# Kernel tuning notes

Measured on AMD Instinct MI355X. Metric: run time of the kernel, lower is better.

## Reference

```python
import jax, jax.numpy as jnp
import numpy as np


def _interp_bilinear_ac(x, out_h, out_w):
    """Bilinear resize with align_corners=True, NCHW."""
    n, c, h, w = x.shape
    ys = jnp.linspace(0.0, h - 1.0, out_h)
    xs = jnp.linspace(0.0, w - 1.0, out_w)
    y0 = jnp.floor(ys).astype(jnp.int32)
    y1 = jnp.minimum(y0 + 1, h - 1)
    wy = (ys - y0.astype(x.dtype))[None, None, :, None]
    x0 = jnp.floor(xs).astype(jnp.int32)
    x1 = jnp.minimum(x0 + 1, w - 1)
    wx = (xs - x0.astype(x.dtype))[None, None, None, :]
    # interpolate along H then W
    xh = x[:, :, y0, :] * (1.0 - wy) + x[:, :, y1, :] * wy  # [n,c,out_h,w]
    out = xh[:, :, :, x0] * (1.0 - wx) + xh[:, :, :, x1] * wx  # [n,c,out_h,out_w]
    return out


def setup_inputs() -> dict:
    key = jax.random.key(0)
    ks = jax.random.split(key, 7)
    return {
        "aspp": jax.random.normal(ks[0], (8, 128, 32, 32), jnp.float32),
        "f3": jax.random.normal(ks[1], (8, 128, 32, 32), jnp.float32),
        "inp": jax.random.normal(ks[2], (8, 4, 512, 512), jnp.float32),
        "cam": jax.random.normal(ks[3], (8, 21, 64, 64), jnp.float32),
        "w_aspp": jax.random.normal(ks[4], (64, 128), jnp.float32) * 0.05,
        "w_f3": jax.random.normal(ks[5], (64, 128), jnp.float32) * 0.05,
        "w_f9": jax.random.normal(ks[6], (128, 132), jnp.float32) * 0.05,
    }


def reference(aspp, f3, inp, cam, w_aspp, w_f3, w_f9):
    n, c, h, w = cam.shape
    # 1x1 convs (no bias) as channel matmuls
    f3p = jnp.einsum('oc,nchw->nohw', w_f3, f3)
    asppp = jnp.einsum('oc,nchw->nohw', w_aspp, aspp)
    # bilinear upsample (align_corners=True) to cam resolution
    asppp = _interp_bilinear_ac(asppp, h, w)
    x_s = _interp_bilinear_ac(inp, h, w)
    f3p = _interp_bilinear_ac(f3p, h, w)
    f = jnp.concatenate([x_s, asppp, f3p], axis=1)  # [n,132,h,w]
    f = jnp.einsum('oc,nchw->nohw', w_f9, f)        # [n,128,h,w]
    f = f.reshape(n, -1, h * w)                     # [n,128,hw]
    f = f / (jnp.linalg.norm(f, axis=1, keepdims=True) + 1e-5)
    # affinity: [n, hw, hw]
    aff = jax.nn.relu(jnp.einsum('ncp,ncq->npq', f, f))
    aff = aff / (jnp.sum(aff, axis=1, keepdims=True) + 1e-5)
    cam_rv = jnp.matmul(cam.reshape(n, -1, h * w), aff).reshape(n, -1, h, w)
    return cam_rv
```

## Files before the change

### kernel.cpp

```cpp
#include <hip/hip_runtime.h>
#include <math.h>

typedef unsigned short u16;
typedef unsigned int u32;
typedef __attribute__((ext_vector_type(8))) short bf16x8;
typedef __attribute__((ext_vector_type(4))) short short4v;
typedef __attribute__((ext_vector_type(4))) float f32x4;
typedef __attribute__((ext_vector_type(16))) float f32x16;

#define HW32 1024
#define HW64 4096
#define KCAM 21
#define PB 64
#define PSPLIT 4
#define FT_STR 168

#define GLOAD_LDS16(gsrc, ldst)                                                \
  __builtin_amdgcn_global_load_lds(                                            \
      (const __attribute__((address_space(1))) void*)(gsrc),                   \
      (__attribute__((address_space(3))) void*)(ldst), 16, 0, 0)

static __device__ __forceinline__ u16 f2bf(float x) {
  u32 u = __float_as_uint(x);
  u32 r = (u + 0x7FFFu + ((u >> 16) & 1u)) >> 16;
  return (u16)r;
}
static __device__ __forceinline__ float bf2f(u16 h) {
  return __uint_as_float(((u32)h) << 16);
}

__global__ __launch_bounds__(256) void k_conv32(
    const float* __restrict__ aspp, const float* __restrict__ f3,
    const float* __restrict__ w_aspp, const float* __restrict__ w_f3,
    const float* __restrict__ w_f9,
    float* __restrict__ a32, float* __restrict__ g32,
    u16* __restrict__ whi, u16* __restrict__ wlo)
{
  const int pt = blockIdx.x, which = blockIdx.y >> 2, jq = blockIdx.y & 3,
            n = blockIdx.z;

  if (blockIdx.y == 0) {
    const int bid = blockIdx.z * 4 + blockIdx.x;
#pragma unroll
    for (int k = 0; k < 3; ++k) {
      const int idx = bid * 256 + threadIdx.x + k * 8192;
      if (idx < 128 * 160) {
        const int o = idx / 160, c = idx - o * 160;
        const float v = (c < 132) ? w_f9[o * 132 + c] : 0.f;
        const u16 h = f2bf(v);
        whi[idx] = h;
        wlo[idx] = f2bf(v - bf2f(h));
      }
    }
  }

  const float* x = (which == 0 ? aspp : f3) + (size_t)n * 128 * HW32;
  const float* w = (which == 0 ? w_aspp : w_f3) + jq * 16 * 128;
  float* out = (which == 0 ? a32 : g32) + (size_t)n * 64 * HW32 + (size_t)jq * 16 * HW32;

  __shared__ __align__(16) float wlds[16 * 128];
  for (int i = threadIdx.x; i < 16 * 128; i += 256) wlds[i] = w[i];
  __syncthreads();

  const int p = pt * 256 + threadIdx.x;
  float acc[16];
#pragma unroll
  for (int j = 0; j < 16; ++j) acc[j] = 0.f;

  for (int c0 = 0; c0 < 128; c0 += 8) {
    float xv[8];
#pragma unroll
    for (int cc = 0; cc < 8; ++cc) xv[cc] = x[(size_t)(c0 + cc) * HW32 + p];
#pragma unroll
    for (int j = 0; j < 16; ++j) {
      const float4 w0 = *reinterpret_cast<const float4*>(&wlds[j * 128 + c0]);
      const float4 w1 = *reinterpret_cast<const float4*>(&wlds[j * 128 + c0 + 4]);
      acc[j] = fmaf(w0.x, xv[0], acc[j]);
      acc[j] = fmaf(w0.y, xv[1], acc[j]);
      acc[j] = fmaf(w0.z, xv[2], acc[j]);
      acc[j] = fmaf(w0.w, xv[3], acc[j]);
      acc[j] = fmaf(w1.x, xv[4], acc[j]);
      acc[j] = fmaf(w1.y, xv[5], acc[j]);
      acc[j] = fmaf(w1.z, xv[6], acc[j]);
      acc[j] = fmaf(w1.w, xv[7], acc[j]);
    }
  }
  for (int j = 0; j < 16; ++j) out[(size_t)j * HW32 + p] = acc[j];
}

__global__ __launch_bounds__(512) void k_build_f(
    const float* __restrict__ inp, const float* __restrict__ a32,
    const float* __restrict__ g32, const u16* __restrict__ whi,
    const u16* __restrict__ wlo, const float* __restrict__ cam,
    u16* __restrict__ fhi_g, u16* __restrict__ camA)
{
  const int y2 = blockIdx.x, n = blockIdx.y;
  const int tid = threadIdx.x;

  __shared__ __align__(16) u16 feat[128 * FT_STR];
  __shared__ __align__(16) u16 wh[128 * FT_STR];
  __shared__ __align__(16) u16 wl[128 * FT_STR];

  for (int ch = tid; ch < 2560; ch += 512) {
    const int o = ch / 20, c8 = (ch - o * 20) * 8;
    *(bf16x8*)&wh[o * FT_STR + c8] = *(const bf16x8*)(whi + o * 160 + c8);
    *(bf16x8*)&wl[o * FT_STR + c8] = *(const bf16x8*)(wlo + o * 160 + c8);
  }

  {
    u16* dst = camA + ((size_t)n * 32 + y2) * HW64;
    if (y2 < KCAM) {
      const float* src = cam + ((size_t)n * KCAM + y2) * HW64;
      for (int i = tid; i < HW64; i += 512) dst[i] = f2bf(src[i]);
    } else {
      const u16 v = (y2 == KCAM) ? f2bf(1.f) : (u16)0;
      for (int i = tid; i < HW64; i += 512) dst[i] = v;
    }
  }

  const float s512 = 511.f / 63.f, s32 = 31.f / 63.f;
  const int yA0i = y2 * 2, yA1i = y2 * 2 + 1;
  const float sA0 = yA0i * s512, sA1 = yA1i * s512;
  const int y0A0 = (int)sA0, y0A1 = (int)sA1;
  const float wyA0 = sA0 - y0A0, wyA1 = sA1 - y0A1;
  const int y1A0 = min(y0A0 + 1, 511), y1A1 = min(y0A1 + 1, 511);
  const float sB0 = yA0i * s32, sB1 = yA1i * s32;
  const int y0B0 = (int)sB0, y0B1 = (int)sB1;
  const float wyB0 = sB0 - y0B0, wyB1 = sB1 - y0B1;
  const int y1B0 = min(y0B0 + 1, 31), y1B1 = min(y0B1 + 1, 31);

  for (int idx = tid; idx < 132 * 128; idx += 512) {
    const int c = idx >> 7;
    const int pos = idx & 127;
    const int ly = pos >> 6, x = pos & 63;
    const int y0A = ly ? y0A1 : y0A0, y1A = ly ? y1A1 : y1A0;
    const float wyA = ly ? wyA1 : wyA0;
    const int y0B = ly ? y0B1 : y0B0, y1B = ly ? y1B1 : y1B0;
    const float wyB = ly ? wyB1 : wyB0;
    float v;
    if (c < 4) {
      const float sx = x * s512;
      const int x0 = (int)sx;
      const float wx = sx - (float)x0;
      const int x1 = min(x0 + 1, 511);
      const float* im = inp + (size_t)(n * 4 + c) * 512 * 512;
      const float v00 = im[y0A * 512 + x0], v01 = im[y0A * 512 + x1];
      const float v10 = im[y1A * 512 + x0], v11 = im[y1A * 512 + x1];
      v = (v00 * (1.f - wx) + v01 * wx) * (1.f - wyA) +
          (v10 * (1.f - wx) + v11 * wx) * wyA;
    } else {
      const float* im = (c < 68) ? a32 + (size_t)(n * 64 + (c - 4)) * HW32
                                 : g32 + (size_t)(n * 64 + (c - 68)) * HW32;
      const float sx = x * s32;
      const int x0 = (int)sx;
      const float wx = sx - (float)x0;
      const int x1 = min(x0 + 1, 31);
      const float v00 = im[y0B * 32 + x0], v01 = im[y0B * 32 + x1];
      const float v10 = im[y1B * 32 + x0], v11 = im[y1B * 32 + x1];
      v = (v00 * (1.f - wx) + v01 * wx) * (1.f - wyB) +
          (v10 * (1.f - wx) + v11 * wx) * wyB;
    }
    feat[pos * FT_STR + c] = f2bf(v);
  }
  for (int idx = tid; idx < 28 * 128; idx += 512) {
    const int c = 132 + (idx >> 7), pos = idx & 127;
    feat[pos * FT_STR + c] = 0;
  }
  __syncthreads();

  const int lane = tid & 63, wave = tid >> 6;
  const int l15 = lane & 15, l4 = lane >> 4;

  float acc[8][4];
#pragma unroll
  for (int m = 0; m < 8; ++m)
#pragma unroll
    for (int i = 0; i < 4; ++i) acc[m][i] = 0.f;

#pragma unroll
  for (int s = 0; s < 5; ++s) {
    const bf16x8 B =
        *(const bf16x8*)&feat[(wave * 16 + l15) * FT_STR + s * 32 + l4 * 8];
#pragma unroll
    for (int m = 0; m < 8; ++m) {
      const int wo = (m * 16 + l15) * FT_STR + s * 32 + l4 * 8;
      const bf16x8 Ahi = *(const bf16x8*)&wh[wo];
      const bf16x8 Alo = *(const bf16x8*)&wl[wo];
      f32x4 a = {acc[m][0], acc[m][1], acc[m][2], acc[m][3]};
      a = __builtin_amdgcn_mfma_f32_16x16x32_bf16(Ahi, B, a, 0, 0, 0);
      a = __builtin_amdgcn_mfma_f32_16x16x32_bf16(Alo, B, a, 0, 0, 0);
      acc[m][0] = a[0]; acc[m][1] = a[1]; acc[m][2] = a[2]; acc[m][3] = a[3];
    }
  }

  {
    float ss = 0.f;
#pragma unroll
    for (int m = 0; m < 8; ++m)
#pragma unroll
      for (int i = 0; i < 4; ++i) ss = fmaf(acc[m][i], acc[m][i], ss);
    ss += __shfl_xor(ss, 16);
    ss += __shfl_xor(ss, 32);
    const float inv = 1.f / (sqrtf(ss) + 1e-5f);
    const int pos = wave * 16 + l15;
    u16* fp = fhi_g + ((size_t)n * HW64 + (size_t)(y2 * 2 + (pos >> 6)) * 64 +
                       (pos & 63)) * 128 + l4 * 4;
#pragma unroll
    for (int m = 0; m < 8; ++m) {
      const float v0 = acc[m][0] * inv, v1 = acc[m][1] * inv;
      const float v2 = acc[m][2] * inv, v3 = acc[m][3] * inv;
      union { u32 d[2]; short4v h; } P;
      asm("v_cvt_pk_bf16_f32 %0, %1, %2" : "=v"(P.d[0]) : "v"(v0), "v"(v1));
      asm("v_cvt_pk_bf16_f32 %0, %1, %2" : "=v"(P.d[1]) : "v"(v2), "v"(v3));
      *(short4v*)(fp + m * 16) = P.h;
    }
  }
}

__global__ __launch_bounds__(256) void k_fused(
    const u16* __restrict__ fhi_g, const u16* __restrict__ camA,
    float* __restrict__ part)
{
  __shared__ __align__(16) u16 fh[2][PB * 128];

  const int gx = blockIdx.x;
  const int n = gx & 7;
  const int rest = gx >> 3;
  const int qt = rest & 15;
  const int ps = rest >> 4;
  const int tid = threadIdx.x;
  const int lane = tid & 63;
  const int wq = tid >> 6;
  const int l31 = lane & 31;
  const int lh = lane >> 5;
  const int qb = qt * 256;

  const u16* fbase = fhi_g + (size_t)n * HW64 * 128;

  bf16x8 Bq[2][8];
#pragma unroll
  for (int qh = 0; qh < 2; ++qh) {
    const size_t rowo = (size_t)(qb + wq * 64 + qh * 32 + l31) * 128;
#pragma unroll
    for (int ks = 0; ks < 8; ++ks)
      Bq[qh][ks] = *(const bf16x8*)(fbase + rowo + ks * 16 + lh * 8);
  }

  f32x16 nacc0, nacc1;
#pragma unroll
  for (int i = 0; i < 16; ++i) { nacc0[i] = 0.f; nacc1[i] = 0.f; }

  const int p_base = ps * (HW64 / PSPLIT);
  const int xorr = (l31 & 7) << 4;

  const int srow0 = (lane >> 4);
  const int scbl = (lane & 15) * 16;

#pragma unroll
  for (int s = 0; s < 4; ++s) {
    const int rr = (wq * 4 + s) * 4 + srow0;
    const u16* gsrc = fbase + (size_t)(p_base + rr) * 128 +
                      ((scbl ^ ((rr & 7) << 4)) >> 1);
    GLOAD_LDS16(gsrc, &fh[0][(wq * 4 + s) * 512]);
  }

  int cur = 0;
  for (int t = 0; t < (HW64 / PSPLIT) / PB; ++t) {
    const int p0 = p_base + t * PB;
    __syncthreads();

    if (t < 15) {
#pragma unroll
      for (int s = 0; s < 4; ++s) {
        const int rr = (wq * 4 + s) * 4 + srow0;
        const u16* gsrc = fbase + (size_t)(p0 + PB + rr) * 128 +
                          ((scbl ^ ((rr & 7) << 4)) >> 1);
        GLOAD_LDS16(gsrc, &fh[cur ^ 1][(wq * 4 + s) * 512]);
      }
    }

    bf16x8 Ac[4];
#pragma unroll
    for (int kst = 0; kst < 4; ++kst) {
      union { short4v h[2]; bf16x8 v; } A;
      const u16* cp = camA + ((size_t)n * 32 + l31) * HW64 + p0 + kst * 16 + lh * 4;
      A.h[0] = *(const short4v*)cp;
      A.h[1] = *(const short4v*)(cp + 8);
      Ac[kst] = A.v;
    }

    f32x16 accS[2][2];
#pragma unroll
    for (int ks = 0; ks < 8; ++ks) {
      const int cb = (ks * 32 + (lh << 4)) ^ xorr;
      bf16x8 Ah[2];
#pragma unroll
      for (int mt = 0; mt < 2; ++mt)
        Ah[mt] = *(const bf16x8*)&fh[cur][(mt * 32 + l31) * 128 + (cb >> 1)];
      if (ks == 0) {
        f32x16 z;
#pragma unroll
        for (int i = 0; i < 16; ++i) z[i] = 0.f;
#pragma unroll
        for (int mt = 0; mt < 2; ++mt) {
          accS[mt][0] = __builtin_amdgcn_mfma_f32_32x32x16_bf16(Ah[mt], Bq[0][0], z, 0, 0, 0);
          accS[mt][1] = __builtin_amdgcn_mfma_f32_32x32x16_bf16(Ah[mt], Bq[1][0], z, 0, 0, 0);
        }
      } else {
#pragma unroll
        for (int mt = 0; mt < 2; ++mt) {
          accS[mt][0] = __builtin_amdgcn_mfma_f32_32x32x16_bf16(Ah[mt], Bq[0][ks], accS[mt][0], 0, 0, 0);
          accS[mt][1] = __builtin_amdgcn_mfma_f32_32x32x16_bf16(Ah[mt], Bq[1][ks], accS[mt][1], 0, 0, 0);
        }
      }
    }

#pragma unroll
    for (int kst = 0; kst < 4; ++kst) {
      const int mt = kst >> 1, h8 = (kst & 1) * 8;
#pragma unroll
      for (int qh = 0; qh < 2; ++qh) {
        union { u32 d[4]; bf16x8 v; } W;
#pragma unroll
        for (int i = 0; i < 4; ++i) {
          const float a0 = fmaxf(accS[mt][qh][h8 + 2 * i], 0.f);
          const float a1 = fmaxf(accS[mt][qh][h8 + 2 * i + 1], 0.f);
          asm("v_cvt_pk_bf16_f32 %0, %1, %2" : "=v"(W.d[i]) : "v"(a0), "v"(a1));
        }
        if (qh == 0)
          nacc0 = __builtin_amdgcn_mfma_f32_32x32x16_bf16(Ac[kst], W.v, nacc0, 0, 0, 0);
        else
          nacc1 = __builtin_amdgcn_mfma_f32_32x32x16_bf16(Ac[kst], W.v, nacc1, 0, 0, 0);
      }
    }

    cur ^= 1;
  }

#pragma unroll
  for (int qh = 0; qh < 2; ++qh) {
    const int qg = qb + wq * 64 + qh * 32 + l31;
#pragma unroll
    for (int r = 0; r < 16; ++r) {
      const int row = (r & 3) + 8 * (r >> 2) + 4 * lh;
      if (row < 22)
        part[(((size_t)n * PSPLIT + ps) * 22 + row) * HW64 + qg] =
            (qh == 0) ? nacc0[r] : nacc1[r];
    }
  }
}

__global__ __launch_bounds__(256) void k_final(
    const float* __restrict__ part, float* __restrict__ out, int total4)
{
  const int idx = blockIdx.x * 256 + threadIdx.x;
  if (idx >= total4) return;
  const int n = idx / (KCAM * 1024);
  const int r = idx - n * (KCAM * 1024);
  const int k = r >> 10;
  const int q4 = (r & 1023) * 4;
  const float* base = part + (size_t)n * PSPLIT * 22 * HW64;
  float4 num = {0.f, 0.f, 0.f, 0.f}, den = {0.f, 0.f, 0.f, 0.f};
#pragma unroll
  for (int p = 0; p < PSPLIT; ++p) {
    const float4 nv = *reinterpret_cast<const float4*>(
        &base[((size_t)p * 22 + k) * HW64 + q4]);
    const float4 dv = *reinterpret_cast<const float4*>(
        &base[((size_t)p * 22 + 21) * HW64 + q4]);
    num.x += nv.x; num.y += nv.y; num.z += nv.z; num.w += nv.w;
    den.x += dv.x; den.y += dv.y; den.z += dv.z; den.w += dv.w;
  }
  float4 o;
  o.x = num.x / (den.x + 1e-5f);
  o.y = num.y / (den.y + 1e-5f);
  o.z = num.z / (den.z + 1e-5f);
  o.w = num.w / (den.w + 1e-5f);
  *reinterpret_cast<float4*>(&out[((size_t)n * KCAM + k) * HW64 + q4]) = o;
}

extern "C" void kernel_launch(void* const* d_in, const int* in_sizes, int n_in,
                              void* d_out, int out_size, void* d_ws, size_t ws_size,
                              hipStream_t stream) {
  const float* aspp   = (const float*)d_in[0];
  const float* f3     = (const float*)d_in[1];
  const float* inp    = (const float*)d_in[2];
  const float* cam    = (const float*)d_in[3];
  const float* w_aspp = (const float*)d_in[4];
  const float* w_f3   = (const float*)d_in[5];
  const float* w_f9   = (const float*)d_in[6];
  float* out = (float*)d_out;

  u16*   fhi  = (u16*)d_ws;
  u16*   camA = fhi + 4194304;
  u16*   whi  = camA + 1048576;
  u16*   wlo  = whi + 20480;
  float* part = (float*)(wlo + 20480);
  float* a32  = part;
  float* g32  = a32 + 524288;

  k_conv32<<<dim3(4, 8, 8), 256, 0, stream>>>(aspp, f3, w_aspp, w_f3, w_f9,
                                              a32, g32, whi, wlo);
  k_build_f<<<dim3(32, 8), 512, 0, stream>>>(inp, a32, g32, whi, wlo, cam,
                                             fhi, camA);
  k_fused<<<512, 256, 0, stream>>>(fhi, camA, part);
  k_final<<<672, 256, 0, stream>>>(part, out, 8 * KCAM * 1024);
}
```

Baseline: 91.24 us.

## Fuse 1x1 convs into build_f using MFMA on needed low-res rows

Removes the separate k_conv32 kernel and computes the aspp/f3 1x1 convolutions inside k_build_f. Each block works only on the (up to 3) low-resolution rows its two output rows need, using split-bf16 MFMA with the intermediate held in LDS as bf16. The w_f9 hi/lo split is also done per block rather than once. This saves one launch and the global round trip of the intermediates, at the cost of recomputing conv rows across neighbouring blocks, extra LDS use (lower occupancy), and bf16 rounding of the conv outputs.

```diff
diff --git a/kernel.cpp b/kernel.cpp
--- a/kernel.cpp
+++ b/kernel.cpp
@@ -14,6 +14,8 @@
 #define PB 64
 #define PSPLIT 4
 #define FT_STR 168
+#define XI_STR 136
+#define C32_STR 104
 
 #define GLOAD_LDS16(gsrc, ldst)                                                \
   __builtin_amdgcn_global_load_lds(                                            \
@@ -29,84 +31,30 @@
   return __uint_as_float(((u32)h) << 16);
 }
 
-__global__ __launch_bounds__(256) void k_conv32(
-    const float* __restrict__ aspp, const float* __restrict__ f3,
-    const float* __restrict__ w_aspp, const float* __restrict__ w_f3,
-    const float* __restrict__ w_f9,
-    float* __restrict__ a32, float* __restrict__ g32,
-    u16* __restrict__ whi, u16* __restrict__ wlo)
-{
-  const int pt = blockIdx.x, which = blockIdx.y >> 2, jq = blockIdx.y & 3,
-            n = blockIdx.z;
-
-  if (blockIdx.y == 0) {
-    const int bid = blockIdx.z * 4 + blockIdx.x;
-#pragma unroll
-    for (int k = 0; k < 3; ++k) {
-      const int idx = bid * 256 + threadIdx.x + k * 8192;
-      if (idx < 128 * 160) {
-        const int o = idx / 160, c = idx - o * 160;
-        const float v = (c < 132) ? w_f9[o * 132 + c] : 0.f;
-        const u16 h = f2bf(v);
-        whi[idx] = h;
-        wlo[idx] = f2bf(v - bf2f(h));
-      }
-    }
-  }
-
-  const float* x = (which == 0 ? aspp : f3) + (size_t)n * 128 * HW32;
-  const float* w = (which == 0 ? w_aspp : w_f3) + jq * 16 * 128;
-  float* out = (which == 0 ? a32 : g32) + (size_t)n * 64 * HW32 + (size_t)jq * 16 * HW32;
-
-  __shared__ __align__(16) float wlds[16 * 128];
-  for (int i = threadIdx.x; i < 16 * 128; i += 256) wlds[i] = w[i];
-  __syncthreads();
-
-  const int p = pt * 256 + threadIdx.x;
-  float acc[16];
-#pragma unroll
-  for (int j = 0; j < 16; ++j) acc[j] = 0.f;
-
-  for (int c0 = 0; c0 < 128; c0 += 8) {
-    float xv[8];
-#pragma unroll
-    for (int cc = 0; cc < 8; ++cc) xv[cc] = x[(size_t)(c0 + cc) * HW32 + p];
-#pragma unroll
-    for (int j = 0; j < 16; ++j) {
-      const float4 w0 = *reinterpret_cast<const float4*>(&wlds[j * 128 + c0]);
-      const float4 w1 = *reinterpret_cast<const float4*>(&wlds[j * 128 + c0 + 4]);
-      acc[j] = fmaf(w0.x, xv[0], acc[j]);
-      acc[j] = fmaf(w0.y, xv[1], acc[j]);
-      acc[j] = fmaf(w0.z, xv[2], acc[j]);
-      acc[j] = fmaf(w0.w, xv[3], acc[j]);
-      acc[j] = fmaf(w1.x, xv[4], acc[j]);
-      acc[j] = fmaf(w1.y, xv[5], acc[j]);
-      acc[j] = fmaf(w1.z, xv[6], acc[j]);
-      acc[j] = fmaf(w1.w, xv[7], acc[j]);
-    }
-  }
-  for (int j = 0; j < 16; ++j) out[(size_t)j * HW32 + p] = acc[j];
-}
-
 __global__ __launch_bounds__(512) void k_build_f(
-    const float* __restrict__ inp, const float* __restrict__ a32,
-    const float* __restrict__ g32, const u16* __restrict__ whi,
-    const u16* __restrict__ wlo, const float* __restrict__ cam,
+    const float* __restrict__ inp, const float* __restrict__ aspp,
+    const float* __restrict__ f3g, const float* __restrict__ w_aspp,
+    const float* __restrict__ w_f3, const float* __restrict__ w_f9,
+    const float* __restrict__ cam,
     u16* __restrict__ fhi_g, u16* __restrict__ camA)
 {
   const int y2 = blockIdx.x, n = blockIdx.y;
   const int tid = threadIdx.x;
 
-  __shared__ __align__(16) u16 feat[128 * FT_STR];
   __shared__ __align__(16) u16 wh[128 * FT_STR];
   __shared__ __align__(16) u16 wl[128 * FT_STR];
-
-  for (int ch = tid; ch < 2560; ch += 512) {
-    const int o = ch / 20, c8 = (ch - o * 20) * 8;
-    *(bf16x8*)&wh[o * FT_STR + c8] = *(const bf16x8*)(whi + o * 160 + c8);
-    *(bf16x8*)&wl[o * FT_STR + c8] = *(const bf16x8*)(wlo + o * 160 + c8);
-  }
-
+  __shared__ __align__(16) u16 featA[128 * FT_STR];
+  __shared__ __align__(16) u16 c32[128 * C32_STR];
+
+  u16* xin = featA;
+
+  for (int e = tid; e < 128 * 160; e += 512) {
+    const int o = e / 160, c = e - o * 160;
+    const float v = (c < 132) ? w_f9[o * 132 + c] : 0.f;
+    const u16 h = f2bf(v);
+    wh[o * FT_STR + c] = h;
+    wl[o * FT_STR + c] = f2bf(v - bf2f(h));
+  }
   {
     u16* dst = camA + ((size_t)n * 32 + y2) * HW64;
     if (y2 < KCAM) {
@@ -129,16 +77,70 @@
   const float wyB0 = sB0 - y0B0, wyB1 = sB1 - y0B1;
   const int y1B0 = min(y0B0 + 1, 31), y1B1 = min(y0B1 + 1, 31);
 
+  const int r0 = y0B0;
+  const int sl0B0 = 0;
+  const int sl1B0 = y1B0 - r0;
+  const int sl0B1 = y0B1 - r0;
+  const int sl1B1 = y1B1 - r0;
+
+  const int lane = tid & 63, wave = tid >> 6;
+  const int l15 = lane & 15, l4 = lane >> 4;
+
+  const int cm = wave & 3, chalf = wave >> 2;
+
+#pragma unroll
+  for (int which = 0; which < 2; ++which) {
+    const float* src = (which == 0 ? aspp : f3g) + (size_t)n * 128 * HW32;
+    const float* wsrc = (which == 0 ? w_aspp : w_f3);
+
+    for (int e = tid; e < 128 * 96; e += 512) {
+      const int ch = e / 96, j = e - ch * 96;
+      const int rr = min(r0 + (j >> 5), 31);
+      xin[j * XI_STR + ch] = f2bf(src[(size_t)ch * HW32 + rr * 32 + (j & 31)]);
+    }
+    __syncthreads();
+
+    f32x4 cacc[3];
+#pragma unroll
+    for (int pt = 0; pt < 3; ++pt) cacc[pt] = {0.f, 0.f, 0.f, 0.f};
+#pragma unroll
+    for (int s = 0; s < 4; ++s) {
+      union { u16 h[8]; bf16x8 v; } Ahi, Alo;
+      const float* wrow = wsrc + (cm * 16 + l15) * 128 + s * 32 + l4 * 8;
+#pragma unroll
+      for (int e = 0; e < 8; ++e) {
+        const float v = wrow[e];
+        const u16 h = f2bf(v);
+        Ahi.h[e] = h;
+        Alo.h[e] = f2bf(v - bf2f(h));
+      }
+#pragma unroll
+      for (int pt = 0; pt < 3; ++pt) {
+        const int px = (chalf * 3 + pt) * 16 + l15;
+        const bf16x8 B = *(const bf16x8*)&xin[px * XI_STR + s * 32 + l4 * 8];
+        cacc[pt] = __builtin_amdgcn_mfma_f32_16x16x32_bf16(Ahi.v, B, cacc[pt], 0, 0, 0);
+        cacc[pt] = __builtin_amdgcn_mfma_f32_16x16x32_bf16(Alo.v, B, cacc[pt], 0, 0, 0);
+      }
+    }
+#pragma unroll
+    for (int pt = 0; pt < 3; ++pt) {
+      const int px = (chalf * 3 + pt) * 16 + l15;
+#pragma unroll
+      for (int i = 0; i < 4; ++i)
+        c32[(which * 64 + cm * 16 + l4 * 4 + i) * C32_STR + px] =
+            f2bf(cacc[pt][i]);
+    }
+    __syncthreads();
+  }
+
   for (int idx = tid; idx < 132 * 128; idx += 512) {
     const int c = idx >> 7;
     const int pos = idx & 127;
     const int ly = pos >> 6, x = pos & 63;
-    const int y0A = ly ? y0A1 : y0A0, y1A = ly ? y1A1 : y1A0;
-    const float wyA = ly ? wyA1 : wyA0;
-    const int y0B = ly ? y0B1 : y0B0, y1B = ly ? y1B1 : y1B0;
-    const float wyB = ly ? wyB1 : wyB0;
     float v;
     if (c < 4) {
+      const int y0A = ly ? y0A1 : y0A0, y1A = ly ? y1A1 : y1A0;
+      const float wyA = ly ? wyA1 : wyA0;
       const float sx = x * s512;
       const int x0 = (int)sx;
       const float wx = sx - (float)x0;
@@ -149,27 +151,28 @@
       v = (v00 * (1.f - wx) + v01 * wx) * (1.f - wyA) +
           (v10 * (1.f - wx) + v11 * wx) * wyA;
     } else {
-      const float* im = (c < 68) ? a32 + (size_t)(n * 64 + (c - 4)) * HW32
-                                 : g32 + (size_t)(n * 64 + (c - 68)) * HW32;
+      const int wh_ = (c < 68) ? 0 : 1;
+      const int cc = (c < 68) ? (c - 4) : (c - 68);
+      const int s0 = ly ? sl0B1 : sl0B0;
+      const int s1 = ly ? sl1B1 : sl1B0;
+      const float wyB = ly ? wyB1 : wyB0;
       const float sx = x * s32;
       const int x0 = (int)sx;
       const float wx = sx - (float)x0;
       const int x1 = min(x0 + 1, 31);
-      const float v00 = im[y0B * 32 + x0], v01 = im[y0B * 32 + x1];
-      const float v10 = im[y1B * 32 + x0], v11 = im[y1B * 32 + x1];
+      const u16* row = &c32[(wh_ * 64 + cc) * C32_STR];
+      const float v00 = bf2f(row[s0 * 32 + x0]), v01 = bf2f(row[s0 * 32 + x1]);
+      const float v10 = bf2f(row[s1 * 32 + x0]), v11 = bf2f(row[s1 * 32 + x1]);
       v = (v00 * (1.f - wx) + v01 * wx) * (1.f - wyB) +
           (v10 * (1.f - wx) + v11 * wx) * wyB;
     }
-    feat[pos * FT_STR + c] = f2bf(v);
+    featA[pos * FT_STR + c] = f2bf(v);
   }
   for (int idx = tid; idx < 28 * 128; idx += 512) {
     const int c = 132 + (idx >> 7), pos = idx & 127;
-    feat[pos * FT_STR + c] = 0;
+    featA[pos * FT_STR + c] = 0;
   }
   __syncthreads();
-
-  const int lane = tid & 63, wave = tid >> 6;
-  const int l15 = lane & 15, l4 = lane >> 4;
 
   float acc[8][4];
 #pragma unroll
@@ -180,7 +183,7 @@
 #pragma unroll
   for (int s = 0; s < 5; ++s) {
     const bf16x8 B =
-        *(const bf16x8*)&feat[(wave * 16 + l15) * FT_STR + s * 32 + l4 * 8];
+        *(const bf16x8*)&featA[(wave * 16 + l15) * FT_STR + s * 32 + l4 * 8];
 #pragma unroll
     for (int m = 0; m < 8; ++m) {
       const int wo = (m * 16 + l15) * FT_STR + s * 32 + l4 * 8;
@@ -392,16 +395,10 @@
 
   u16*   fhi  = (u16*)d_ws;
   u16*   camA = fhi + 4194304;
-  u16*   whi  = camA + 1048576;
-  u16*   wlo  = whi + 20480;
-  float* part = (float*)(wlo + 20480);
-  float* a32  = part;
-  float* g32  = a32 + 524288;
-
-  k_conv32<<<dim3(4, 8, 8), 256, 0, stream>>>(aspp, f3, w_aspp, w_f3, w_f9,
-                                              a32, g32, whi, wlo);
-  k_build_f<<<dim3(32, 8), 512, 0, stream>>>(inp, a32, g32, whi, wlo, cam,
-                                             fhi, camA);
+  float* part = (float*)(camA + 1048576);
+
+  k_build_f<<<dim3(32, 8), 512, 0, stream>>>(inp, aspp, f3, w_aspp, w_f3,
+                                             w_f9, cam, fhi, camA);
   k_fused<<<512, 256, 0, stream>>>(fhi, camA, part);
   k_final<<<672, 256, 0, stream>>>(part, out, 8 * KCAM * 1024);
 }
```

New measurement: 90.57 us. Within noise of the previous version (-0.7%).
